# Performance work log

Hardware: AMD Instinct MI355X
Metric: run time of the kernel (lower is better)

## Reference

```python
import jax, jax.numpy as jnp
import numpy as np

N_NODES = 100_000
E_OFF = 1_000_000
HID = 32
GF = 8
NF = 8
N_LAYERS = 3


def _mlp(h, W1, b1, W2, b2):
    # Linear -> ReLU -> Linear (matches MLP([in, hidden, out]))
    return jax.nn.relu(h @ W1 + b1) @ W2 + b2


def _seg_mean(v, idx, n):
    s = jax.ops.segment_sum(v, idx, num_segments=n)
    c = jax.ops.segment_sum(jnp.ones((v.shape[0], 1), v.dtype), idx, num_segments=n)
    return s / jnp.maximum(c, 1.0)


def _graphnet(x, row, col, eattr2, g, p):
    # GraphNet with global block: edge MLP -> mean-aggregate to nodes -> node MLP -> global MLP
    eW1, eb1, eW2, eb2, nW1, nb1, nW2, nb2, gW1, gb1, gW2, gb2 = p
    n, e = x.shape[0], row.shape[0]
    gE = jnp.broadcast_to(g, (e, g.shape[1]))
    e_emb = _mlp(jnp.concatenate([gE, x[row], x[col], eattr2], axis=1), eW1, eb1, eW2, eb2)
    agg = _seg_mean(e_emb, row, n)
    gN = jnp.broadcast_to(g, (n, g.shape[1]))
    n_emb = _mlp(jnp.concatenate([gN, x, agg], axis=1), nW1, nb1, nW2, nb2)
    g_new = _mlp(jnp.concatenate([n_emb.mean(0, keepdims=True), e_emb.mean(0, keepdims=True), g], axis=1),
                 gW1, gb1, gW2, gb2)
    return e_emb, n_emb, g_new


def setup_inputs() -> dict:
    key = jax.random.key(0)
    ks = jax.random.split(key, 24)
    a = jax.random.randint(ks[0], (E_OFF,), 0, N_NODES)
    b = jax.random.randint(ks[1], (E_OFF,), 0, N_NODES)
    d = jnp.arange(N_NODES)
    l_ei = jnp.stack([jnp.concatenate([jnp.maximum(a, b), d]),
                      jnp.concatenate([jnp.minimum(a, b), d])])  # lower triangular + diag
    c = jax.random.randint(ks[2], (E_OFF,), 0, N_NODES)
    e = jax.random.randint(ks[3], (E_OFF,), 0, N_NODES)
    u_ei = jnp.stack([jnp.concatenate([jnp.minimum(c, e), d]),
                      jnp.concatenate([jnp.maximum(c, e), d])])  # upper triangular + diag
    E = E_OFF + N_NODES
    x = jax.random.normal(ks[4], (N_NODES, NF), dtype=jnp.float32)
    l_attr = jax.random.normal(ks[5], (E, 1), dtype=jnp.float32)
    u_attr = jax.random.normal(ks[6], (E, 1), dtype=jnp.float32)

    def w(k, shape):
        return (jax.random.normal(k, shape, dtype=jnp.float32) / np.sqrt(shape[-2])).astype(jnp.float32)

    e_in = GF + 2 * NF + 1 + 1  # 26 (edge attr padded to 2: skip col, zeros where absent)
    n_in = GF + 1 + NF          # 17
    g_in = NF + 1 + GF          # 17
    return {
        'x': x, 'l_edge_index': l_ei, 'u_edge_index': u_ei,
        'l_edge_attr': l_attr, 'u_edge_attr': u_attr,
        'eW1': w(ks[7], (2, N_LAYERS, e_in, HID)), 'eb1': 0.01 * jax.random.normal(ks[8], (2, N_LAYERS, HID)),
        'eW2': w(ks[9], (2, N_LAYERS, HID, 1)), 'eb2': 0.01 * jax.random.normal(ks[10], (2, N_LAYERS, 1)),
        'nW1': w(ks[11], (2, N_LAYERS, n_in, HID)), 'nb1': 0.01 * jax.random.normal(ks[12], (2, N_LAYERS, HID)),
        'nW2': w(ks[13], (2, N_LAYERS, HID, NF)), 'nb2': 0.01 * jax.random.normal(ks[14], (2, N_LAYERS, NF)),
        'gW1': w(ks[15], (2, N_LAYERS, g_in, HID)), 'gb1': 0.01 * jax.random.normal(ks[16], (2, N_LAYERS, HID)),
        'gW2': w(ks[17], (2, N_LAYERS, HID, GF)), 'gb2': 0.01 * jax.random.normal(ks[18], (2, N_LAYERS, GF)),
    }


def reference(x, l_edge_index, u_edge_index, l_edge_attr, u_edge_attr,
              eW1, eb1, eW2, eb2, nW1, nb1, nW2, nb2, gW1, gb1, gW2, gb2):
    params = (eW1, eb1, eW2, eb2, nW1, nb1, nW2, nb2, gW1, gb1, gW2, gb2)
    lr, lc = l_edge_index[0], l_edge_index[1]
    ur, uc = u_edge_index[0], u_edge_index[1]
    g = jnp.zeros((1, GF), x.dtype)
    l_e, u_e = l_edge_attr, u_edge_attr
    l_a = l_edge_attr  # skip-connection edge features (original matrix values)
    zl, zu = jnp.zeros_like(l_edge_attr), jnp.zeros_like(u_edge_attr)
    for i in range(N_LAYERS):
        p1 = tuple(w[0, i] for w in params)
        p2 = tuple(w[1, i] for w in params)
        l_in = jnp.concatenate([l_e, l_a if i != 0 else zl], axis=1)  # zeros col == no skip (block 0)
        l_e, l_n, g = _graphnet(x, lr, lc, l_in, g, p1)
        u_in = jnp.concatenate([u_e, zu], axis=1)  # l2 never has skip; padded zeros col
        u_e, u_n, g = _graphnet(l_n, ur, uc, u_in, g, p2)
        # NOTE: node embeddings are NOT carried across MP blocks in the original
    l_vals = jnp.where(lr == lc, jnp.exp(l_e[:, 0]), l_e[:, 0])
    u_vals = jnp.where(ur == uc, jnp.exp(u_e[:, 0]), u_e[:, 0])
    return jnp.concatenate([l_vals, u_vals])
```

## Files before the change

kernel.cpp:

```cpp
#include <hip/hip_runtime.h>


typedef unsigned int u32;

#define NB_SHIFT 8
#define NB_SIZE 256
#define RSTRIDE 1104

__device__ __forceinline__ float wave_sum(float v) {
#pragma unroll
    for (int off = 32; off > 0; off >>= 1) v += __shfl_down(v, off, 64);
    return v;
}


__global__ __launch_bounds__(512) void hist_kernel(
    const int* __restrict__ lr, const int* __restrict__ ur,
    u32* __restrict__ hist, int E, int B) {
    __shared__ u32 h[512];
    const int t = threadIdx.x;
    if (t < B) h[t] = 0;
    __syncthreads();
    const int s = blockIdx.y;
    const int* rows = s ? ur : lr;
    for (int i = blockIdx.x * 512 + t; i < E; i += gridDim.x * 512)
        atomicAdd(&h[rows[i] >> NB_SHIFT], 1u);
    __syncthreads();
    if (t < B && h[t]) atomicAdd(&hist[s * B + t], h[t]);
}

__global__ __launch_bounds__(512) void scan_kernel(
    const u32* __restrict__ hist, u32* __restrict__ offs,
    u32* __restrict__ cur, int B) {
    __shared__ u32 sh[512];
    const int t = threadIdx.x;
    for (int s = 0; s < 2; ++s) {
        const u32 v = (t < B) ? hist[s * B + t] : 0u;
        sh[t] = v;
        __syncthreads();
#pragma unroll
        for (int off = 1; off < 512; off <<= 1) {
            const u32 add = (t >= off) ? sh[t - off] : 0u;
            __syncthreads();
            sh[t] += add;
            __syncthreads();
        }
        const u32 exc = sh[t] - v;
        if (t < B) {
            offs[s * (B + 1) + t] = exc;
            cur[s * B + t] = exc;
        }
        if (t == 511) offs[s * (B + 1) + B] = sh[511];
        __syncthreads();
    }
}

#define SCHUNK 4096
__global__ __launch_bounds__(512) void scatter_kernel(
    const int* __restrict__ lr, const int* __restrict__ lc,
    const int* __restrict__ ur, const int* __restrict__ uc,
    const float* __restrict__ la, const float* __restrict__ ua,
    u32* __restrict__ cur, uint4* __restrict__ einfo, int E, int B) {
    __shared__ u32 lcnt[512], lbase[512];
    const int t = threadIdx.x;
    const int s = blockIdx.y;
    const int* rows = s ? ur : lr;
    const int* cols = s ? uc : lc;
    const float* attr = s ? ua : la;
    uint4* my = einfo + (size_t)s * E;
    if (t < B) lcnt[t] = 0;
    __syncthreads();
    const int base_e = blockIdx.x * SCHUNK;
#pragma unroll
    for (int k = 0; k < SCHUNK / 512; ++k) {
        const int e = base_e + k * 512 + t;
        if (e < E) atomicAdd(&lcnt[rows[e] >> NB_SHIFT], 1u);
    }
    __syncthreads();
    if (t < B) {
        const u32 c = lcnt[t];
        lbase[t] = c ? atomicAdd(&cur[s * B + t], c) : 0u;
        lcnt[t] = 0;
    }
    __syncthreads();
#pragma unroll
    for (int k = 0; k < SCHUNK / 512; ++k) {
        const int e = base_e + k * 512 + t;
        if (e < E) {
            const int r = rows[e];
            const int b = r >> NB_SHIFT;
            const u32 pos = lbase[b] + atomicAdd(&lcnt[b], 1u);
            my[pos] = make_uint4((u32)r, (u32)cols[e], (u32)e,
                                 __float_as_uint(attr[e]));
        }
    }
}


template <bool GCOMP>
__global__ __launch_bounds__(256) void nodew_kernel(
    const float4* __restrict__ xf, const float* __restrict__ W1,
    const float* __restrict__ b1,
    const float* __restrict__ gprev,
    float* __restrict__ gout,
    const float* __restrict__ pebins,
    const float* __restrict__ pnbins,
    const float* __restrict__ gW1, const float* __restrict__ gb1,
    const float* __restrict__ gW2, const float* __restrict__ gb2,
    float4* __restrict__ Atab, int N, float inv_E) {
    __shared__ float gsh[8];
    const int t = threadIdx.x;
    if constexpr (GCOMP) {
        if (t < 64) {
            float nb[8];
#pragma unroll
            for (int q = 0; q < 8; ++q) nb[q] = pnbins[t * 16 + q];
            const float eb = pebins[t];
            float gin[17];
#pragma unroll
            for (int q = 0; q < 8; ++q) {
                const float s = wave_sum(nb[q]);
                gin[q] = __shfl(s, 0, 64) / (float)N;
            }
            const float es = wave_sum(eb);
            gin[8] = __shfl(es, 0, 64) * inv_E;
#pragma unroll
            for (int k = 0; k < 8; ++k) gin[9 + k] = gprev[k];
            float hv = 0.0f;
            if (t < 32) {
                hv = gb1[t];
#pragma unroll
                for (int k = 0; k < 17; ++k)
                    hv = fmaf(gin[k], gW1[k * 32 + t], hv);
                hv = fmaxf(hv, 0.0f);
            }
#pragma unroll
            for (int q = 0; q < 8; ++q) {
                const float c = (t < 32) ? hv * gW2[t * 8 + q] : 0.0f;
                const float s = wave_sum(c);
                if (t == 0) {
                    const float gv = gb2[q] + s;
                    gsh[q] = gv;
                    if (blockIdx.x == 0) gout[q] = gv;
                }
            }
        }
    } else {
        if (t < 8) gsh[t] = gprev[t];
    }
    __syncthreads();
    const int n = blockIdx.x * 256 + t;
    if (n >= N) return;
    float gr[8];
#pragma unroll
    for (int k = 0; k < 8; ++k) gr[k] = gsh[k];
    const float4 x0 = xf[2 * (size_t)n], x1 = xf[2 * (size_t)n + 1];
    const float xs[8] = {x0.x, x0.y, x0.z, x0.w, x1.x, x1.y, x1.z, x1.w};
    float a[32];
#pragma unroll
    for (int j = 0; j < 32; ++j) {
        float v = b1[j];
#pragma unroll
        for (int k = 0; k < 8; ++k) v = fmaf(gr[k], W1[k * 32 + j], v);
        a[j] = v;
    }
    const float* __restrict__ WA = W1 + 8 * 32;
#pragma unroll
    for (int k = 0; k < 8; ++k) {
        const float v = xs[k];
#pragma unroll
        for (int j = 0; j < 32; ++j) a[j] = fmaf(v, WA[k * 32 + j], a[j]);
    }
    float4* An = Atab + 8 * (size_t)n;
#pragma unroll
    for (int q = 0; q < 8; ++q)
        An[q] = make_float4(a[4 * q], a[4 * q + 1], a[4 * q + 2], a[4 * q + 3]);
}


template <bool SKIP, bool FIRST, bool GAGG, bool VALS, bool STORE>
__global__ __launch_bounds__(256) void edge_kernel(
    const uint4* __restrict__ einfo,
    const float4* __restrict__ Atab,
    const float4* __restrict__ xf,
    const float* __restrict__ eprev,
    const float* __restrict__ W1,
    const float* __restrict__ W2,
    const float* __restrict__ b2,
    float* __restrict__ ebins,
    float* __restrict__ e_out,
    float* __restrict__ vals_out,
    int E, int cpx) {
    __shared__ float wpart[4];
    const int t = threadIdx.x;
    const int lid = (blockIdx.x & 7) * cpx + (blockIdx.x >> 3);
    const int i0 = lid * 256;
    if (i0 >= E) return;
    const int i = i0 + t;
    const bool valid = i < E;
    const int idx = valid ? i : i0;

    const uint4 e4 = einfo[idx];
    const float attr = __uint_as_float(e4.w);
    float epv;
    if constexpr (FIRST) epv = attr;
    else epv = eprev[idx];
    const float4* __restrict__ Ar = Atab + 8 * (size_t)e4.x;
    float h[32];
#pragma unroll
    for (int q = 0; q < 8; ++q) {
        const float4 av = Ar[q];
        h[4 * q + 0] = av.x; h[4 * q + 1] = av.y;
        h[4 * q + 2] = av.z; h[4 * q + 3] = av.w;
    }
    const float4 xc0 = xf[2 * (size_t)e4.y], xc1 = xf[2 * (size_t)e4.y + 1];
    const float cx[8] = {xc0.x, xc0.y, xc0.z, xc0.w,
                         xc1.x, xc1.y, xc1.z, xc1.w};
    const float* __restrict__ Wc = W1 + 16 * 32;
#pragma unroll
    for (int k = 0; k < 8; ++k) {
        const float v = cx[k];
#pragma unroll
        for (int j = 0; j < 32; ++j) h[j] = fmaf(v, Wc[k * 32 + j], h[j]);
    }
    const float* __restrict__ W24 = W1 + 24 * 32;
#pragma unroll
    for (int j = 0; j < 32; ++j) h[j] = fmaf(epv, W24[j], h[j]);
    if constexpr (SKIP) {
        const float* __restrict__ W25 = W1 + 25 * 32;
#pragma unroll
        for (int j = 0; j < 32; ++j) h[j] = fmaf(attr, W25[j], h[j]);
    }
    float out = b2[0];
#pragma unroll
    for (int j = 0; j < 32; ++j) out = fmaf(fmaxf(h[j], 0.0f), W2[j], out);

    if (valid) {
        if constexpr (STORE) e_out[i] = out;
        if constexpr (VALS)
            vals_out[e4.z] = (e4.x == e4.y) ? expf(out) : out;
    }
    if constexpr (GAGG) {
        const float s = wave_sum(valid ? out : 0.0f);
        if ((t & 63) == 0) wpart[t >> 6] = s;
        __syncthreads();
        if (t == 0)
            atomicAdd(&ebins[lid & 63],
                      wpart[0] + wpart[1] + wpart[2] + wpart[3]);
    }
}


template <bool COUNT, bool STORE_N>
__global__ __launch_bounds__(512) void aggnode_kernel(
    const float* __restrict__ ep,
    const uint4* __restrict__ einfo,
    const u32* __restrict__ offs,
    const float4* __restrict__ xf,
    float* __restrict__ cntf,
    const float* __restrict__ g,
    const float* __restrict__ nW1, const float* __restrict__ nb1,
    const float* __restrict__ nW2, const float* __restrict__ nb2,
    float* __restrict__ n_out,
    float* __restrict__ nbins,
    int N) {
    __shared__ float sbin[NB_SIZE];
    __shared__ float cbin[NB_SIZE];
    __shared__ float biasN[32];
    __shared__ float npart[4][8];
    const int t = threadIdx.x;
    if (t < NB_SIZE) {
        sbin[t] = 0.0f;
        if constexpr (COUNT) cbin[t] = 0.0f;
    }
    if (t >= NB_SIZE && t < NB_SIZE + 32) {
        const int j = t - NB_SIZE;
        float v = nb1[j];
#pragma unroll
        for (int k = 0; k < 8; ++k) v = fmaf(g[k], nW1[k * 32 + j], v);
        biasN[j] = v;
    }
    __syncthreads();
    const int b = blockIdx.x;
    const u32 beg = offs[b], end = offs[b + 1];
    for (u32 i = beg + t; i < end; i += 512) {
        const float v = ep[i];
        const u32 rl = einfo[i].x & (NB_SIZE - 1);
        atomicAdd(&sbin[rl], v);
        if constexpr (COUNT) atomicAdd(&cbin[rl], 1.0f);
    }
    __syncthreads();

    const int n0 = b << NB_SHIFT;
    float o[8];
    const bool active = (t < NB_SIZE) && (n0 + t < N);
    if (t < NB_SIZE) {
        const int n = n0 + t;
        const int idx = active ? n : (N - 1);
        float cntv;
        if constexpr (COUNT) {
            cntv = cbin[t];
            if (active) cntf[n] = cntv;
        } else {
            cntv = cntf[idx];
        }
        const float agg = sbin[t] / fmaxf(cntv, 1.0f);
        const float4 x0 = xf[2 * idx], x1 = xf[2 * idx + 1];
        float in[9] = {x0.x, x0.y, x0.z, x0.w, x1.x, x1.y, x1.z, x1.w, agg};
        float h[32];
#pragma unroll
        for (int j = 0; j < 8; ++j) {
            const float4 bb = reinterpret_cast<const float4*>(biasN)[j];
            h[4 * j + 0] = bb.x; h[4 * j + 1] = bb.y;
            h[4 * j + 2] = bb.z; h[4 * j + 3] = bb.w;
        }
        const float* __restrict__ Wk = nW1 + 8 * 32;
#pragma unroll
        for (int k = 0; k < 9; ++k) {
            const float v = in[k];
#pragma unroll
            for (int j = 0; j < 32; ++j) h[j] = fmaf(v, Wk[k * 32 + j], h[j]);
        }
#pragma unroll
        for (int q = 0; q < 8; ++q) o[q] = nb2[q];
#pragma unroll
        for (int j = 0; j < 32; ++j) {
            const float hv = fmaxf(h[j], 0.0f);
#pragma unroll
            for (int q = 0; q < 8; ++q) o[q] = fmaf(hv, nW2[j * 8 + q], o[q]);
        }
        if constexpr (STORE_N) {
            if (active) {
                reinterpret_cast<float4*>(n_out)[2 * n] =
                    make_float4(o[0], o[1], o[2], o[3]);
                reinterpret_cast<float4*>(n_out)[2 * n + 1] =
                    make_float4(o[4], o[5], o[6], o[7]);
            }
        }
#pragma unroll
        for (int q = 0; q < 8; ++q) {
            const float s = wave_sum(active ? o[q] : 0.0f);
            if ((t & 63) == 0) npart[t >> 6][q] = s;
        }
    }
    __syncthreads();
    if (t < 8) {
        float a = 0.0f;
#pragma unroll
        for (int w = 0; w < 4; ++w) a += npart[w][t];
        atomicAdd(&nbins[(b & 63) * 16 + t], a);
    }
}

extern "C" void kernel_launch(void* const* d_in, const int* in_sizes, int n_in,
                              void* d_out, int out_size, void* d_ws,
                              size_t ws_size, hipStream_t stream) {
    const float* x = (const float*)d_in[0];
    const int* l_ei = (const int*)d_in[1];
    const int* u_ei = (const int*)d_in[2];
    const float* l_attr = (const float*)d_in[3];
    const float* u_attr = (const float*)d_in[4];
    const float* eW1 = (const float*)d_in[5];
    const float* eb1 = (const float*)d_in[6];
    const float* eW2 = (const float*)d_in[7];
    const float* eb2 = (const float*)d_in[8];
    const float* nW1 = (const float*)d_in[9];
    const float* nb1 = (const float*)d_in[10];
    const float* nW2 = (const float*)d_in[11];
    const float* nb2 = (const float*)d_in[12];
    const float* gW1 = (const float*)d_in[13];
    const float* gb1 = (const float*)d_in[14];
    const float* gW2 = (const float*)d_in[15];
    const float* gb2 = (const float*)d_in[16];

    const int E = in_sizes[3];
    const int N = in_sizes[0] / 8;
    const int B = (N + NB_SIZE - 1) >> NB_SHIFT;
    const int Ep = (E + 3) & ~3;

    uint4* einfo = (uint4*)d_ws;
    float* Atab = (float*)(einfo + (size_t)2 * E);
    float* l_e = Atab + (size_t)32 * N;
    float* u_e = l_e + Ep;
    float* l_n = u_e + Ep;
    float* cnt_l = l_n + (size_t)8 * N;
    float* cnt_u = cnt_l + N;
    float* gslot = cnt_u + N;
    u32* hist = (u32*)(gslot + 56);
    float* dyn_all = (float*)(hist + 2 * B);
    u32* offs = (u32*)(dyn_all + 5 * RSTRIDE);
    u32* cur = offs + 2 * (B + 1);

    const int* lr = l_ei;
    const int* lc = l_ei + E;
    const int* ur = u_ei;
    const int* uc = u_ei + E;
    const int sg = (E + SCHUNK - 1) / SCHUNK;
    const int ng = (N + 255) / 256;
    const int eg = (E + 255) / 256;
    const int nwg8 = (eg + 7) & ~7;
    const int cpx = nwg8 >> 3;
    const float invE = 1.0f / (float)E;
    float* outL = (float*)d_out;
    float* outU = outL + E;
    const u32* offs_l = offs;
    const u32* offs_u = offs + (B + 1);

    hipMemsetAsync(gslot, 0, (size_t)(56 + 2 * B + 5 * RSTRIDE) * sizeof(float),
                   stream);
    hist_kernel<<<dim3(64, 2), 512, 0, stream>>>(lr, ur, hist, E, B);
    scan_kernel<<<1, 512, 0, stream>>>(hist, offs, cur, B);
    scatter_kernel<<<dim3(sg, 2), 512, 0, stream>>>(lr, lc, ur, uc, l_attr,
                                                    u_attr, cur, einfo, E, B);

    const size_t wsl[6] = {0, 3, 1, 4, 2, 5};

    for (int j = 0; j < 6; ++j) {
        const bool lower = !(j & 1);
        const size_t sl = wsl[j];
        float* ebins = dyn_all + (size_t)(j <= 4 ? j : 4) * RSTRIDE;
        float* nbins = ebins + 64;
        const float* pe = (j >= 1) ? dyn_all + (size_t)(j - 1) * RSTRIDE : nullptr;
        const float* pn = (j >= 1) ? pe + 64 : nullptr;
        const size_t psl = (j >= 1) ? wsl[j - 1] : 0;
        const float4* exf = (const float4*)(lower ? x : l_n);
        const uint4* einfo_t = einfo + (size_t)(lower ? 0 : 1) * E;
        const u32* eoffs = lower ? offs_l : offs_u;
        const float* eprev = lower ? l_e : u_e;
        float* e_out = lower ? l_e : u_e;
        const float* gprev = gslot + (size_t)(j >= 1 ? j - 1 : 0) * 8;
        float* gout = gslot + (size_t)j * 8;

        if (j == 0)
            nodew_kernel<false><<<ng, 256, 0, stream>>>(
                exf, eW1 + sl * 832, eb1 + sl * 32, gprev, gout, pe, pn,
                gW1, gb1, gW2, gb2, (float4*)Atab, N, invE);
        else
            nodew_kernel<true><<<ng, 256, 0, stream>>>(
                exf, eW1 + sl * 832, eb1 + sl * 32, gprev, gout, pe, pn,
                gW1 + psl * 544, gb1 + psl * 32, gW2 + psl * 256,
                gb2 + psl * 8, (float4*)Atab, N, invE);

#define EDGE_ARGS                                                             \
    einfo_t, (const float4*)Atab, exf, eprev, eW1 + sl * 832,                 \
        eW2 + sl * 32, eb2 + sl, ebins, e_out, (j == 4) ? outL : outU, E, cpx

        switch (j) {
            case 0: edge_kernel<false, true, true, false, true>
                        <<<nwg8, 256, 0, stream>>>(EDGE_ARGS); break;
            case 1: edge_kernel<false, true, true, false, true>
                        <<<nwg8, 256, 0, stream>>>(EDGE_ARGS); break;
            case 2: edge_kernel<true, false, true, false, true>
                        <<<nwg8, 256, 0, stream>>>(EDGE_ARGS); break;
            case 3: edge_kernel<false, false, true, false, true>
                        <<<nwg8, 256, 0, stream>>>(EDGE_ARGS); break;
            case 4: edge_kernel<true, false, true, true, true>
                        <<<nwg8, 256, 0, stream>>>(EDGE_ARGS); break;
            case 5: edge_kernel<false, false, false, true, false>
                        <<<nwg8, 256, 0, stream>>>(EDGE_ARGS); break;
        }
#undef EDGE_ARGS

        if (j == 5) break;

        float* cntf = lower ? cnt_l : cnt_u;
        const float4* nxf = (const float4*)(lower ? x : l_n);

#define AGG_ARGS                                                              \
    e_out, einfo_t, eoffs, nxf, cntf, gslot + (size_t)j * 8, nW1 + sl * 544,  \
        nb1 + sl * 32, nW2 + sl * 256, nb2 + sl * 8, l_n, nbins, N

        switch (j) {
            case 0: aggnode_kernel<true, true>
                        <<<B, 512, 0, stream>>>(AGG_ARGS); break;
            case 1: aggnode_kernel<true, false>
                        <<<B, 512, 0, stream>>>(AGG_ARGS); break;
            case 2: aggnode_kernel<false, true>
                        <<<B, 512, 0, stream>>>(AGG_ARGS); break;
            case 3: aggnode_kernel<false, false>
                        <<<B, 512, 0, stream>>>(AGG_ARGS); break;
            case 4: aggnode_kernel<false, true>
                        <<<B, 512, 0, stream>>>(AGG_ARGS); break;
        }
#undef AGG_ARGS
    }
}
```

Measured before the change: 549.5 us.

## Fuse segment-sum into edge kernel via global atomics, replace aggnode with node MLP

The edge kernel now adds each edge output (and on the first pass a count) straight into per-node global sums with atomics. This replaces the separate aggregation pass, which re-read the edge outputs and edge info sorted by row bucket and summed them in shared memory. A simpler per-node MLP kernel then reads and clears the sums. The change removes one full pass over edge data per layer, but adds about 1.1M global float atomics per edge launch, which can contend on high-degree nodes and makes the summation order nondeterministic.

```diff
diff --git a/kernel.cpp b/kernel.cpp
--- a/kernel.cpp
+++ b/kernel.cpp
@@ -178,7 +178,8 @@
 }
 
 
-template <bool SKIP, bool FIRST, bool GAGG, bool VALS, bool STORE>
+template <bool SKIP, bool FIRST, bool GAGG, bool VALS, bool STORE, bool NAGG,
+          bool COUNT>
 __global__ __launch_bounds__(256) void edge_kernel(
     const uint4* __restrict__ einfo,
     const float4* __restrict__ Atab,
@@ -190,6 +191,8 @@
     float* __restrict__ ebins,
     float* __restrict__ e_out,
     float* __restrict__ vals_out,
+    float* __restrict__ nsum,
+    float* __restrict__ ncnt,
     int E, int cpx) {
     __shared__ float wpart[4];
     const int t = threadIdx.x;
@@ -239,6 +242,10 @@
         if constexpr (STORE) e_out[i] = out;
         if constexpr (VALS)
             vals_out[e4.z] = (e4.x == e4.y) ? expf(out) : out;
+        if constexpr (NAGG) {
+            atomicAdd(&nsum[e4.x], out);
+            if constexpr (COUNT) atomicAdd(&ncnt[e4.x], 1.0f);
+        }
     }
     if constexpr (GAGG) {
         const float s = wave_sum(valid ? out : 0.0f);
@@ -251,104 +258,77 @@
 }
 
 
-template <bool COUNT, bool STORE_N>
-__global__ __launch_bounds__(512) void aggnode_kernel(
-    const float* __restrict__ ep,
-    const uint4* __restrict__ einfo,
-    const u32* __restrict__ offs,
+template <bool STORE_N>
+__global__ __launch_bounds__(256) void nodemlp_kernel(
+    float* __restrict__ nsum,
+    const float* __restrict__ cntf,
     const float4* __restrict__ xf,
-    float* __restrict__ cntf,
     const float* __restrict__ g,
     const float* __restrict__ nW1, const float* __restrict__ nb1,
     const float* __restrict__ nW2, const float* __restrict__ nb2,
     float* __restrict__ n_out,
     float* __restrict__ nbins,
     int N) {
-    __shared__ float sbin[NB_SIZE];
-    __shared__ float cbin[NB_SIZE];
     __shared__ float biasN[32];
     __shared__ float npart[4][8];
     const int t = threadIdx.x;
-    if (t < NB_SIZE) {
-        sbin[t] = 0.0f;
-        if constexpr (COUNT) cbin[t] = 0.0f;
-    }
-    if (t >= NB_SIZE && t < NB_SIZE + 32) {
-        const int j = t - NB_SIZE;
-        float v = nb1[j];
-#pragma unroll
-        for (int k = 0; k < 8; ++k) v = fmaf(g[k], nW1[k * 32 + j], v);
-        biasN[j] = v;
-    }
-    __syncthreads();
-    const int b = blockIdx.x;
-    const u32 beg = offs[b], end = offs[b + 1];
-    for (u32 i = beg + t; i < end; i += 512) {
-        const float v = ep[i];
-        const u32 rl = einfo[i].x & (NB_SIZE - 1);
-        atomicAdd(&sbin[rl], v);
-        if constexpr (COUNT) atomicAdd(&cbin[rl], 1.0f);
-    }
-    __syncthreads();
-
-    const int n0 = b << NB_SHIFT;
+    if (t < 32) {
+        float v = nb1[t];
+#pragma unroll
+        for (int k = 0; k < 8; ++k) v = fmaf(g[k], nW1[k * 32 + t], v);
+        biasN[t] = v;
+    }
+    __syncthreads();
+    const int n = blockIdx.x * 256 + t;
+    const bool active = n < N;
+    const int idx = active ? n : (N - 1);
+    const float s = nsum[idx];
+    if (active) nsum[idx] = 0.0f;
+    const float agg = s / fmaxf(cntf[idx], 1.0f);
+    const float4 x0 = xf[2 * (size_t)idx], x1 = xf[2 * (size_t)idx + 1];
+    float in[9] = {x0.x, x0.y, x0.z, x0.w, x1.x, x1.y, x1.z, x1.w, agg};
+    float h[32];
+#pragma unroll
+    for (int j = 0; j < 8; ++j) {
+        const float4 bb = reinterpret_cast<const float4*>(biasN)[j];
+        h[4 * j + 0] = bb.x; h[4 * j + 1] = bb.y;
+        h[4 * j + 2] = bb.z; h[4 * j + 3] = bb.w;
+    }
+    const float* __restrict__ Wk = nW1 + 8 * 32;
+#pragma unroll
+    for (int k = 0; k < 9; ++k) {
+        const float v = in[k];
+#pragma unroll
+        for (int j = 0; j < 32; ++j) h[j] = fmaf(v, Wk[k * 32 + j], h[j]);
+    }
     float o[8];
-    const bool active = (t < NB_SIZE) && (n0 + t < N);
-    if (t < NB_SIZE) {
-        const int n = n0 + t;
-        const int idx = active ? n : (N - 1);
-        float cntv;
-        if constexpr (COUNT) {
-            cntv = cbin[t];
-            if (active) cntf[n] = cntv;
-        } else {
-            cntv = cntf[idx];
-        }
-        const float agg = sbin[t] / fmaxf(cntv, 1.0f);
-        const float4 x0 = xf[2 * idx], x1 = xf[2 * idx + 1];
-        float in[9] = {x0.x, x0.y, x0.z, x0.w, x1.x, x1.y, x1.z, x1.w, agg};
-        float h[32];
-#pragma unroll
-        for (int j = 0; j < 8; ++j) {
-            const float4 bb = reinterpret_cast<const float4*>(biasN)[j];
-            h[4 * j + 0] = bb.x; h[4 * j + 1] = bb.y;
-            h[4 * j + 2] = bb.z; h[4 * j + 3] = bb.w;
-        }
-        const float* __restrict__ Wk = nW1 + 8 * 32;
-#pragma unroll
-        for (int k = 0; k < 9; ++k) {
-            const float v = in[k];
-#pragma unroll
-            for (int j = 0; j < 32; ++j) h[j] = fmaf(v, Wk[k * 32 + j], h[j]);
-        }
-#pragma unroll
-        for (int q = 0; q < 8; ++q) o[q] = nb2[q];
-#pragma unroll
-        for (int j = 0; j < 32; ++j) {
-            const float hv = fmaxf(h[j], 0.0f);
-#pragma unroll
-            for (int q = 0; q < 8; ++q) o[q] = fmaf(hv, nW2[j * 8 + q], o[q]);
-        }
-        if constexpr (STORE_N) {
-            if (active) {
-                reinterpret_cast<float4*>(n_out)[2 * n] =
-                    make_float4(o[0], o[1], o[2], o[3]);
-                reinterpret_cast<float4*>(n_out)[2 * n + 1] =
-                    make_float4(o[4], o[5], o[6], o[7]);
-            }
-        }
-#pragma unroll
-        for (int q = 0; q < 8; ++q) {
-            const float s = wave_sum(active ? o[q] : 0.0f);
-            if ((t & 63) == 0) npart[t >> 6][q] = s;
-        }
+#pragma unroll
+    for (int q = 0; q < 8; ++q) o[q] = nb2[q];
+#pragma unroll
+    for (int j = 0; j < 32; ++j) {
+        const float hv = fmaxf(h[j], 0.0f);
+#pragma unroll
+        for (int q = 0; q < 8; ++q) o[q] = fmaf(hv, nW2[j * 8 + q], o[q]);
+    }
+    if constexpr (STORE_N) {
+        if (active) {
+            reinterpret_cast<float4*>(n_out)[2 * n] =
+                make_float4(o[0], o[1], o[2], o[3]);
+            reinterpret_cast<float4*>(n_out)[2 * n + 1] =
+                make_float4(o[4], o[5], o[6], o[7]);
+        }
+    }
+#pragma unroll
+    for (int q = 0; q < 8; ++q) {
+        const float s2 = wave_sum(active ? o[q] : 0.0f);
+        if ((t & 63) == 0) npart[t >> 6][q] = s2;
     }
     __syncthreads();
     if (t < 8) {
         float a = 0.0f;
 #pragma unroll
         for (int w = 0; w < 4; ++w) a += npart[w][t];
-        atomicAdd(&nbins[(b & 63) * 16 + t], a);
+        atomicAdd(&nbins[(blockIdx.x & 63) * 16 + t], a);
     }
 }
 
@@ -385,7 +365,9 @@
     float* l_n = u_e + Ep;
     float* cnt_l = l_n + (size_t)8 * N;
     float* cnt_u = cnt_l + N;
-    float* gslot = cnt_u + N;
+    float* nsum_l = cnt_u + N;
+    float* nsum_u = nsum_l + N;
+    float* gslot = nsum_u + N;
     u32* hist = (u32*)(gslot + 56);
     float* dyn_all = (float*)(hist + 2 * B);
     u32* offs = (u32*)(dyn_all + 5 * RSTRIDE);
@@ -403,10 +385,9 @@
     const float invE = 1.0f / (float)E;
     float* outL = (float*)d_out;
     float* outU = outL + E;
-    const u32* offs_l = offs;
-    const u32* offs_u = offs + (B + 1);
-
-    hipMemsetAsync(gslot, 0, (size_t)(56 + 2 * B + 5 * RSTRIDE) * sizeof(float),
+
+    hipMemsetAsync(cnt_l, 0,
+                   (size_t)(4 * N + 56 + 2 * B + 5 * RSTRIDE) * sizeof(float),
                    stream);
     hist_kernel<<<dim3(64, 2), 512, 0, stream>>>(lr, ur, hist, E, B);
     scan_kernel<<<1, 512, 0, stream>>>(hist, offs, cur, B);
@@ -425,9 +406,10 @@
         const size_t psl = (j >= 1) ? wsl[j - 1] : 0;
         const float4* exf = (const float4*)(lower ? x : l_n);
         const uint4* einfo_t = einfo + (size_t)(lower ? 0 : 1) * E;
-        const u32* eoffs = lower ? offs_l : offs_u;
         const float* eprev = lower ? l_e : u_e;
         float* e_out = lower ? l_e : u_e;
+        float* nsum = lower ? nsum_l : nsum_u;
+        float* cntf = lower ? cnt_l : cnt_u;
         const float* gprev = gslot + (size_t)(j >= 1 ? j - 1 : 0) * 8;
         float* gout = gslot + (size_t)j * 8;
 
@@ -443,45 +425,45 @@
 
 #define EDGE_ARGS                                                             \
     einfo_t, (const float4*)Atab, exf, eprev, eW1 + sl * 832,                 \
-        eW2 + sl * 32, eb2 + sl, ebins, e_out, (j == 4) ? outL : outU, E, cpx
+        eW2 + sl * 32, eb2 + sl, ebins, e_out, (j == 4) ? outL : outU,        \
+        nsum, cntf, E, cpx
 
         switch (j) {
-            case 0: edge_kernel<false, true, true, false, true>
-                        <<<nwg8, 256, 0, stream>>>(EDGE_ARGS); break;
-            case 1: edge_kernel<false, true, true, false, true>
-                        <<<nwg8, 256, 0, stream>>>(EDGE_ARGS); break;
-            case 2: edge_kernel<true, false, true, false, true>
-                        <<<nwg8, 256, 0, stream>>>(EDGE_ARGS); break;
-            case 3: edge_kernel<false, false, true, false, true>
-                        <<<nwg8, 256, 0, stream>>>(EDGE_ARGS); break;
-            case 4: edge_kernel<true, false, true, true, true>
-                        <<<nwg8, 256, 0, stream>>>(EDGE_ARGS); break;
-            case 5: edge_kernel<false, false, false, true, false>
+            case 0: edge_kernel<false, true, true, false, true, true, true>
+                        <<<nwg8, 256, 0, stream>>>(EDGE_ARGS); break;
+            case 1: edge_kernel<false, true, true, false, true, true, true>
+                        <<<nwg8, 256, 0, stream>>>(EDGE_ARGS); break;
+            case 2: edge_kernel<true, false, true, false, true, true, false>
+                        <<<nwg8, 256, 0, stream>>>(EDGE_ARGS); break;
+            case 3: edge_kernel<false, false, true, false, true, true, false>
+                        <<<nwg8, 256, 0, stream>>>(EDGE_ARGS); break;
+            case 4: edge_kernel<true, false, true, true, true, true, false>
+                        <<<nwg8, 256, 0, stream>>>(EDGE_ARGS); break;
+            case 5: edge_kernel<false, false, false, true, false, false, false>
                         <<<nwg8, 256, 0, stream>>>(EDGE_ARGS); break;
         }
 #undef EDGE_ARGS
 
         if (j == 5) break;
 
-        float* cntf = lower ? cnt_l : cnt_u;
         const float4* nxf = (const float4*)(lower ? x : l_n);
 
-#define AGG_ARGS                                                              \
-    e_out, einfo_t, eoffs, nxf, cntf, gslot + (size_t)j * 8, nW1 + sl * 544,  \
-        nb1 + sl * 32, nW2 + sl * 256, nb2 + sl * 8, l_n, nbins, N
+#define NODE_ARGS                                                             \
+    nsum, cntf, nxf, gslot + (size_t)j * 8, nW1 + sl * 544, nb1 + sl * 32,    \
+        nW2 + sl * 256, nb2 + sl * 8, l_n, nbins, N
 
         switch (j) {
-            case 0: aggnode_kernel<true, true>
-                        <<<B, 512, 0, stream>>>(AGG_ARGS); break;
-            case 1: aggnode_kernel<true, false>
-                        <<<B, 512, 0, stream>>>(AGG_ARGS); break;
-            case 2: aggnode_kernel<false, true>
-                        <<<B, 512, 0, stream>>>(AGG_ARGS); break;
-            case 3: aggnode_kernel<false, false>
-                        <<<B, 512, 0, stream>>>(AGG_ARGS); break;
-            case 4: aggnode_kernel<false, true>
-                        <<<B, 512, 0, stream>>>(AGG_ARGS); break;
-        }
-#undef AGG_ARGS
-    }
-}
+            case 0: nodemlp_kernel<true>
+                        <<<ng, 256, 0, stream>>>(NODE_ARGS); break;
+            case 1: nodemlp_kernel<false>
+                        <<<ng, 256, 0, stream>>>(NODE_ARGS); break;
+            case 2: nodemlp_kernel<true>
+                        <<<ng, 256, 0, stream>>>(NODE_ARGS); break;
+            case 3: nodemlp_kernel<false>
+                        <<<ng, 256, 0, stream>>>(NODE_ARGS); break;
+            case 4: nodemlp_kernel<true>
+                        <<<ng, 256, 0, stream>>>(NODE_ARGS); break;
+        }
+#undef NODE_ARGS
+    }
+}
```

New measurement: 695.1 us. 26.5% more time.
